# Kernel tuning notes

Hardware: AMD Instinct MI355X
Metric: run time of the kernel (lower is better)

## Reference

```python
import jax, jax.numpy as jnp
import numpy as np

B, S, D, H, F = 4, 2048, 1024, 16, 4096
HD = D // H
EPS = 1e-5


def _xavier(key, shape, fan_in, fan_out):
    a = float(np.sqrt(6.0 / (fan_in + fan_out)))
    return jax.random.uniform(key, shape, jnp.float32, -a, a)


def setup_inputs() -> dict:
    key = jax.random.key(0)
    ks = jax.random.split(key, 8)
    x = jax.random.normal(ks[0], (B, S, D), jnp.float32)
    # torch xavier_uniform on (1,H,D,HD) uses fan_in=D, fan_out=HD
    Wq = _xavier(ks[1], (H, D, HD), D, HD)
    Wk = _xavier(ks[2], (H, D, HD), D, HD)
    Wv = _xavier(ks[3], (H, D, HD), D, HD)
    Wo = _xavier(ks[4], (D, D), D, D)
    w_in = _xavier(ks[5], (D, F), D, F)
    b_in = jnp.zeros((F,), jnp.float32)
    w_out = _xavier(ks[6], (F, D), F, D)
    b_out = jnp.zeros((D,), jnp.float32)
    g1 = jnp.ones((D,), jnp.float32)
    be1 = jnp.zeros((D,), jnp.float32)
    g2 = jnp.ones((D,), jnp.float32)
    be2 = jnp.zeros((D,), jnp.float32)
    return {"x": x, "Wq": Wq, "Wk": Wk, "Wv": Wv, "Wo": Wo,
            "g1": g1, "be1": be1, "w_in": w_in, "b_in": b_in,
            "w_out": w_out, "b_out": b_out, "g2": g2, "be2": be2}


def _layernorm(x, g, b):
    mu = jnp.mean(x, axis=-1, keepdims=True)
    var = jnp.mean(jnp.square(x - mu), axis=-1, keepdims=True)
    return (x - mu) * jax.lax.rsqrt(var + EPS) * g + b


def reference(x, Wq, Wk, Wv, Wo, g1, be1, w_in, b_in, w_out, b_out, g2, be2):
    b, s, d = x.shape
    h, _, hd = Wq.shape
    q = jnp.einsum('bsd,hde->bhse', x, Wq)
    k = jnp.einsum('bsd,hde->bhse', x, Wk)
    v = jnp.einsum('bsd,hde->bhse', x, Wv)
    scores = jnp.einsum('bhse,bhte->bhst', q, k) / jnp.sqrt(jnp.float32(hd))
    causal = jnp.triu(jnp.ones((s, s), bool), k=1)  # [S,S]
    scores = jnp.where(causal, -jnp.inf, scores)
    p = jax.nn.softmax(scores, axis=-1)
    attn = jnp.einsum('bhst,bhte->bhse', p, v)
    # torch .view on contiguous (B,H,S,hd) -> (B,S,H*hd): plain reshape (no transpose)
    attn = attn.reshape(b, s, h * hd)
    attn = attn @ Wo
    x = _layernorm(x + attn, g1, be1)
    ffn = jax.nn.relu(x @ w_in + b_in) @ w_out + b_out
    x = _layernorm(x + ffn, g2, be2)
    return x
```

## Files before the change

### kernel.cpp

```cpp
#include <hip/hip_runtime.h>
#include <hip/hip_bf16.h>

typedef __hip_bfloat16 bf16;

#define BB 4
#define SS 2048
#define DD 1024
#define HH 16
#define FF 4096
#define HD 64
#define LN_EPS 1e-5f
#define QSCALE 0.1803368801111204f

typedef __attribute__((ext_vector_type(8))) __bf16 bf16x8;
typedef __attribute__((ext_vector_type(8))) unsigned short u16x8;
typedef __attribute__((ext_vector_type(4))) float f32x4;

__device__ __forceinline__ float cvt(float v) { return v; }
__device__ __forceinline__ float cvt(bf16 v) { return __bfloat162float(v); }
__device__ __forceinline__ void stf(float* p, float v) { *p = v; }
__device__ __forceinline__ void stf(bf16* p, float v) { *p = __float2bfloat16(v); }

__device__ __forceinline__ unsigned short f2bf_rne(float x) {
    unsigned int u = __float_as_uint(x);
    unsigned int r = (u + 0x7fffu + ((u >> 16) & 1u)) >> 16;
    return (unsigned short)r;
}

__device__ __forceinline__ void async_cp16(const void* g, void* l) {
    __builtin_amdgcn_global_load_lds(
        (const __attribute__((address_space(1))) unsigned int*)g,
        (__attribute__((address_space(3))) unsigned int*)l, 16, 0, 0);
}

__device__ __forceinline__ u16x8 ld_f32_chunk(const float* p) {
    const float4* q = (const float4*)p;
    const float4 a = q[0], b = q[1];
    u16x8 r;
    r[0] = f2bf_rne(a.x); r[1] = f2bf_rne(a.y); r[2] = f2bf_rne(a.z); r[3] = f2bf_rne(a.w);
    r[4] = f2bf_rne(b.x); r[5] = f2bf_rne(b.y); r[6] = f2bf_rne(b.z); r[7] = f2bf_rne(b.w);
    return r;
}

template <typename TA, typename TC, int EPI>
__launch_bounds__(256)
__global__ void mfma_gemm(const TA* __restrict__ A, const bf16* __restrict__ Bt,
                          TC* __restrict__ C, const float* __restrict__ bias,
                          const bf16* __restrict__ resb,
                          bf16* __restrict__ C2, bf16* __restrict__ C3,
                          int M, int N, int K, float oscale) {
    constexpr bool AF = (sizeof(TA) == 4);
    __shared__ unsigned short As[128 * 64];
    __shared__ unsigned short Bs[128 * 64];

    const int tid = threadIdx.x;
    const int lane = tid & 63;
    const int w = tid >> 6;
    const int wm = w >> 1, wn = w & 1;
    const int m0 = blockIdx.y * 128, n0 = blockIdx.x * 128;

    int ff[4], fr[4], fc[4], fg[4];
#pragma unroll
    for (int i = 0; i < 4; ++i) {
        ff[i] = tid + i * 256;
        fr[i] = ff[i] >> 3;
        fc[i] = ff[i] & 7;
        fg[i] = fc[i] ^ (fr[i] & 7);
    }

    f32x4 acc[4][4];
#pragma unroll
    for (int i = 0; i < 4; ++i)
#pragma unroll
        for (int j = 0; j < 4; ++j) acc[i][j] = (f32x4){0.f, 0.f, 0.f, 0.f};

    u16x8 sa[4];
    if (AF) {
#pragma unroll
        for (int i = 0; i < 4; ++i)
            sa[i] = ld_f32_chunk((const float*)A + (size_t)(m0 + fr[i]) * K + fg[i] * 8);
    }

    for (int k0 = 0; k0 < K; k0 += 64) {
        if (k0 > 0) __syncthreads();
        if (AF) {
#pragma unroll
            for (int i = 0; i < 4; ++i)
                *(u16x8*)&As[ff[i] * 8] = sa[i];
        } else {
#pragma unroll
            for (int i = 0; i < 4; ++i)
                async_cp16((const unsigned short*)A + (size_t)(m0 + fr[i]) * K + k0 + fg[i] * 8,
                           &As[ff[i] * 8]);
        }
#pragma unroll
        for (int i = 0; i < 4; ++i)
            async_cp16((const unsigned short*)Bt + (size_t)(n0 + fr[i]) * K + k0 + fg[i] * 8,
                       &Bs[ff[i] * 8]);
        __syncthreads();

        if (AF && k0 + 64 < K) {
            const int kn = k0 + 64;
#pragma unroll
            for (int i = 0; i < 4; ++i)
                sa[i] = ld_f32_chunk((const float*)A + (size_t)(m0 + fr[i]) * K + kn + fg[i] * 8);
        }

#pragma unroll
        for (int ks = 0; ks < 2; ++ks) {
            bf16x8 af[4], bfr[4];
#pragma unroll
            for (int i = 0; i < 4; ++i) {
                const int row = wm * 64 + i * 16 + (lane & 15);
                const int col = wn * 64 + i * 16 + (lane & 15);
                const int g = ks * 4 + (lane >> 4);
                af[i]  = *(const bf16x8*)&As[row * 64 + (g ^ (row & 7)) * 8];
                bfr[i] = *(const bf16x8*)&Bs[col * 64 + (g ^ (col & 7)) * 8];
            }
#pragma unroll
            for (int i = 0; i < 4; ++i)
#pragma unroll
                for (int j = 0; j < 4; ++j)
                    acc[i][j] = __builtin_amdgcn_mfma_f32_16x16x32_bf16(
                        af[i], bfr[j], acc[i][j], 0, 0, 0);
        }
    }

#pragma unroll
    for (int i = 0; i < 4; ++i) {
        const int mrow0 = m0 + wm * 64 + i * 16 + (lane >> 4) * 4;
#pragma unroll
        for (int j = 0; j < 4; ++j) {
            const int n = n0 + wn * 64 + j * 16 + (lane & 15);
            if (EPI == 5) {
                const int reg = n >> 10;
                const int nn = n & 1023;
                if (reg == 0) {
#pragma unroll
                    for (int r = 0; r < 4; ++r)
                        stf((bf16*)C + (size_t)(mrow0 + r) * 1024 + nn, acc[i][j][r] * oscale);
                } else if (reg == 1) {
#pragma unroll
                    for (int r = 0; r < 4; ++r)
                        stf(C2 + (size_t)(mrow0 + r) * 1024 + nn, acc[i][j][r]);
                } else {
                    const int bb = mrow0 >> 11, s = mrow0 & 2047;
                    ushort4 pk;
                    pk.x = f2bf_rne(acc[i][j][0]);
                    pk.y = f2bf_rne(acc[i][j][1]);
                    pk.z = f2bf_rne(acc[i][j][2]);
                    pk.w = f2bf_rne(acc[i][j][3]);
                    *(ushort4*)((unsigned short*)C3 + ((size_t)bb * 1024 + nn) * SS + s) = pk;
                }
            } else {
#pragma unroll
                for (int r = 0; r < 4; ++r) {
                    const size_t idx = (size_t)(mrow0 + r) * N + n;
                    float v = acc[i][j][r];
                    if (EPI == 0) v *= oscale;
                    if (EPI == 2) { v += bias[n]; v = fmaxf(v, 0.0f); }
                    if (EPI == 6) v += bias[n] + cvt(resb[idx]);
                    if (EPI == 7) v += cvt(resb[idx]);
                    stf(&C[idx], v);
                }
            }
        }
    }
}

__launch_bounds__(256)
__global__ void tr_f32_bf16(const float* __restrict__ in, bf16* __restrict__ out,
                            int R, int C) {
    __shared__ float t[32][33];
    const size_t zo = (size_t)blockIdx.z * R * C;
    const int bx = blockIdx.x * 32;
    const int by = blockIdx.y * 32;
    const int tx = threadIdx.x & 31, ty = threadIdx.x >> 5;
#pragma unroll
    for (int i = 0; i < 32; i += 8)
        t[ty + i][tx] = in[zo + (size_t)(by + ty + i) * C + bx + tx];
    __syncthreads();
#pragma unroll
    for (int i = 0; i < 32; i += 8)
        out[zo + (size_t)(bx + ty + i) * R + by + tx] = __float2bfloat16(t[tx][ty + i]);
}

__launch_bounds__(256)
__global__ void f32_to_bf16_kernel(const float* __restrict__ in, bf16* __restrict__ out) {
    const int i = blockIdx.x * 256 + threadIdx.x;
    const float4 v = ((const float4*)in)[i];
    ushort4 p;
    p.x = f2bf_rne(v.x); p.y = f2bf_rne(v.y); p.z = f2bf_rne(v.z); p.w = f2bf_rne(v.w);
    ((ushort4*)out)[i] = p;
}

__launch_bounds__(256, 4)
__global__ void attn_mfma(const bf16* __restrict__ Q, const bf16* __restrict__ K,
                          const bf16* __restrict__ VT, bf16* __restrict__ O) {
    __shared__ unsigned short Ks[64 * 64];
    __shared__ unsigned short Vs[64 * 64];
    __shared__ unsigned short Ps[64 * 72];

    const int tid = threadIdx.x;
    const int lane = tid & 63;
    const int w = tid >> 6;
    const int ln = lane & 15;
    const int qd = lane >> 4;
    const int bh = blockIdx.x;
    const int b = bh >> 4;
    const int h = bh & 15;
    const int qi = 31 - blockIdx.y;
    const int q0 = qi * 64;

    bf16x8 aq[2];
    {
        const unsigned short* qp =
            (const unsigned short*)Q + ((size_t)b * SS + q0 + w * 16 + ln) * DD + h * HD;
#pragma unroll
        for (int ks = 0; ks < 2; ++ks)
            aq[ks] = *(const bf16x8*)(qp + ks * 32 + qd * 8);
    }

    int sf[2], sr[2], sg[2];
#pragma unroll
    for (int i = 0; i < 2; ++i) {
        sf[i] = tid + i * 256;
        sr[i] = sf[i] >> 3;
        sg[i] = (sf[i] & 7) ^ (sr[i] & 7);
    }
    const unsigned short* kbase = (const unsigned short*)K + (size_t)b * SS * DD + h * HD;
    const unsigned short* vbase = (const unsigned short*)VT + (size_t)(b * DD + h * HD) * SS;

    f32x4 oacc[4];
#pragma unroll
    for (int e = 0; e < 4; ++e) oacc[e] = (f32x4){0.f, 0.f, 0.f, 0.f};
    float l_r[4] = {0.f, 0.f, 0.f, 0.f};

    for (int kt = 0; kt <= qi; ++kt) {
        const int t0 = kt * 64;
        __syncthreads();
#pragma unroll
        for (int i = 0; i < 2; ++i) {
            async_cp16(kbase + (size_t)(t0 + sr[i]) * DD + sg[i] * 8, &Ks[sf[i] * 8]);
            async_cp16(vbase + (size_t)sr[i] * SS + t0 + sg[i] * 8, &Vs[sf[i] * 8]);
        }
        __syncthreads();

        f32x4 sfr[4];
#pragma unroll
        for (int ct = 0; ct < 4; ++ct) {
            const int row = ct * 16 + ln;
            const bf16x8 b0 = *(const bf16x8*)&Ks[row * 64 + ((qd) ^ (row & 7)) * 8];
            const bf16x8 b1 = *(const bf16x8*)&Ks[row * 64 + ((4 + qd) ^ (row & 7)) * 8];
            f32x4 t = __builtin_amdgcn_mfma_f32_16x16x32_bf16(
                aq[0], b0, (f32x4){0.f, 0.f, 0.f, 0.f}, 0, 0, 0);
            sfr[ct] = __builtin_amdgcn_mfma_f32_16x16x32_bf16(aq[1], b1, t, 0, 0, 0);
        }

        if (kt == qi) {
#pragma unroll
            for (int ct = 0; ct < 4; ++ct) {
                const int tg = t0 + ct * 16 + ln;
#pragma unroll
                for (int r = 0; r < 4; ++r) {
                    const int qg = q0 + w * 16 + qd * 4 + r;
                    if (tg > qg) sfr[ct][r] = -1e30f;
                }
            }
        }

#pragma unroll
        for (int ct = 0; ct < 4; ++ct)
#pragma unroll
            for (int r = 0; r < 4; ++r)
                sfr[ct][r] = __builtin_amdgcn_exp2f(sfr[ct][r]);
#pragma unroll
        for (int r = 0; r < 4; ++r)
            l_r[r] += (sfr[0][r] + sfr[1][r]) + (sfr[2][r] + sfr[3][r]);

#pragma unroll
        for (int ct = 0; ct < 4; ++ct)
#pragma unroll
            for (int r = 0; r < 4; ++r)
                Ps[(w * 16 + qd * 4 + r) * 72 + ct * 16 + ln] = f2bf_rne(sfr[ct][r]);
        const bf16x8 ap0 = *(const bf16x8*)&Ps[(w * 16 + ln) * 72 + qd * 8];
        const bf16x8 ap1 = *(const bf16x8*)&Ps[(w * 16 + ln) * 72 + 32 + qd * 8];

#pragma unroll
        for (int et = 0; et < 4; ++et) {
            const int row = et * 16 + ln;
            const bf16x8 v0 = *(const bf16x8*)&Vs[row * 64 + ((qd) ^ (row & 7)) * 8];
            const bf16x8 v1 = *(const bf16x8*)&Vs[row * 64 + ((4 + qd) ^ (row & 7)) * 8];
            oacc[et] = __builtin_amdgcn_mfma_f32_16x16x32_bf16(ap0, v0, oacc[et], 0, 0, 0);
            oacc[et] = __builtin_amdgcn_mfma_f32_16x16x32_bf16(ap1, v1, oacc[et], 0, 0, 0);
        }
    }

#pragma unroll
    for (int st = 1; st <= 8; st <<= 1)
#pragma unroll
        for (int r = 0; r < 4; ++r)
            l_r[r] += __shfl_xor(l_r[r], st);
    float linv[4];
#pragma unroll
    for (int r = 0; r < 4; ++r) linv[r] = 1.0f / l_r[r];
    unsigned short* ob = (unsigned short*)O + (size_t)bh * SS * HD;
#pragma unroll
    for (int et = 0; et < 4; ++et)
#pragma unroll
        for (int r = 0; r < 4; ++r) {
            const int qg = q0 + w * 16 + qd * 4 + r;
            ob[(size_t)qg * HD + et * 16 + ln] = f2bf_rne(oacc[et][r] * linv[r]);
        }
}

template <typename TIN, typename TOUT>
__launch_bounds__(256)
__global__ void ln_kernel(const TIN* __restrict__ X, TOUT* __restrict__ Y,
                          const float* __restrict__ g, const float* __restrict__ be) {
    const int row = blockIdx.x;
    const int tid = threadIdx.x;
    const int lane = tid & 63, w = tid >> 6;
    __shared__ float red[8];
    __shared__ float mv[2];

    float4 v;
    if (sizeof(TIN) == 4) {
        v = ((const float4*)((const float*)X + (size_t)row * DD))[tid];
    } else {
        const ushort4 u = ((const ushort4*)((const unsigned short*)X + (size_t)row * DD))[tid];
        v.x = __uint_as_float((unsigned)u.x << 16);
        v.y = __uint_as_float((unsigned)u.y << 16);
        v.z = __uint_as_float((unsigned)u.z << 16);
        v.w = __uint_as_float((unsigned)u.w << 16);
    }
    float s = (v.x + v.y) + (v.z + v.w);
    float q = (v.x * v.x + v.y * v.y) + (v.z * v.z + v.w * v.w);
#pragma unroll
    for (int st = 1; st < 64; st <<= 1) {
        s += __shfl_xor(s, st);
        q += __shfl_xor(q, st);
    }
    if (lane == 0) { red[w] = s; red[4 + w] = q; }
    __syncthreads();
    if (tid == 0) {
        const float ts = (red[0] + red[1]) + (red[2] + red[3]);
        const float tq = (red[4] + red[5]) + (red[6] + red[7]);
        const float mu = ts * (1.0f / DD);
        mv[0] = mu;
        mv[1] = rsqrtf(tq * (1.0f / DD) - mu * mu + LN_EPS);
    }
    __syncthreads();
    const float mu = mv[0], rs = mv[1];
    const float4 gg = ((const float4*)g)[tid];
    const float4 bb = ((const float4*)be)[tid];
    float o[4];
    o[0] = (v.x - mu) * rs * gg.x + bb.x;
    o[1] = (v.y - mu) * rs * gg.y + bb.y;
    o[2] = (v.z - mu) * rs * gg.z + bb.z;
    o[3] = (v.w - mu) * rs * gg.w + bb.w;
    if (sizeof(TOUT) == 4) {
        float4 of = {o[0], o[1], o[2], o[3]};
        ((float4*)((float*)Y + (size_t)row * DD))[tid] = of;
    } else {
        ushort4 p;
        p.x = f2bf_rne(o[0]); p.y = f2bf_rne(o[1]);
        p.z = f2bf_rne(o[2]); p.w = f2bf_rne(o[3]);
        ((ushort4*)((unsigned short*)Y + (size_t)row * DD))[tid] = p;
    }
}

extern "C" void kernel_launch(void* const* d_in, const int* in_sizes, int n_in,
                              void* d_out, int out_size, void* d_ws, size_t ws_size,
                              hipStream_t stream) {
    const float* x = (const float*)d_in[0];
    const float* Wq = (const float*)d_in[1];
    const float* Wk = (const float*)d_in[2];
    const float* Wv = (const float*)d_in[3];
    const float* Wo = (const float*)d_in[4];
    const float* g1 = (const float*)d_in[5];
    const float* be1 = (const float*)d_in[6];
    const float* w_in = (const float*)d_in[7];
    const float* b_in = (const float*)d_in[8];
    const float* w_out = (const float*)d_in[9];
    const float* b_out = (const float*)d_in[10];
    const float* g2 = (const float*)d_in[11];
    const float* be2 = (const float*)d_in[12];
    float* out = (float*)d_out;

    char* wsb = (char*)d_ws;
    const size_t MiB = 1u << 20;
    bf16* Qb = (bf16*)(wsb);
    bf16* Kb = (bf16*)(wsb + 16 * MiB);
    bf16* VT = (bf16*)(wsb + 32 * MiB);
    bf16* At = (bf16*)(wsb + 48 * MiB);
    bf16* xb = (bf16*)(wsb + 64 * MiB);
    bf16* X1b = (bf16*)(wsb + 80 * MiB);
    bf16* Hd = (bf16*)(wsb);
    bf16* X2b = (bf16*)(wsb + 64 * MiB);
    bf16* WqkvT = (bf16*)(wsb + 96 * MiB);
    bf16* WoT = (bf16*)(wsb + 102 * MiB);
    bf16* w_inT = (bf16*)(wsb + 104 * MiB);
    bf16* w_outT = (bf16*)(wsb + 112 * MiB);
    (void)ws_size;

    const int M = BB * SS;
    dim3 blk(256);

    f32_to_bf16_kernel<<<dim3(M * DD / 4 / 256), blk, 0, stream>>>(x, xb);

    tr_f32_bf16<<<dim3(2, 32, 16), blk, 0, stream>>>(Wq, WqkvT, DD, HD);
    tr_f32_bf16<<<dim3(2, 32, 16), blk, 0, stream>>>(Wk, WqkvT + (size_t)DD * DD, DD, HD);
    tr_f32_bf16<<<dim3(2, 32, 16), blk, 0, stream>>>(Wv, WqkvT + 2 * (size_t)DD * DD, DD, HD);
    tr_f32_bf16<<<dim3(32, 32, 1), blk, 0, stream>>>(Wo, WoT, DD, DD);
    tr_f32_bf16<<<dim3(128, 32, 1), blk, 0, stream>>>(w_in, w_inT, DD, FF);
    tr_f32_bf16<<<dim3(32, 128, 1), blk, 0, stream>>>(w_out, w_outT, FF, DD);

    mfma_gemm<bf16, bf16, 5><<<dim3(3 * DD / 128, M / 128), blk, 0, stream>>>(
        xb, WqkvT, Qb, nullptr, nullptr, Kb, VT, M, 3 * DD, DD, QSCALE);

    attn_mfma<<<dim3(BB * HH, SS / 64), blk, 0, stream>>>(Qb, Kb, VT, At);

    mfma_gemm<bf16, bf16, 7><<<dim3(DD / 128, M / 128), blk, 0, stream>>>(
        At, WoT, X1b, nullptr, xb, nullptr, nullptr, M, DD, DD, 1.0f);
    ln_kernel<bf16, bf16><<<dim3(M), blk, 0, stream>>>(X1b, X1b, g1, be1);

    mfma_gemm<bf16, bf16, 2><<<dim3(FF / 128, M / 128), blk, 0, stream>>>(
        X1b, w_inT, Hd, b_in, nullptr, nullptr, nullptr, M, FF, DD, 1.0f);

    mfma_gemm<bf16, bf16, 6><<<dim3(DD / 128, M / 128), blk, 0, stream>>>(
        Hd, w_outT, X2b, b_out, X1b, nullptr, nullptr, M, DD, FF, 1.0f);

    ln_kernel<bf16, float><<<dim3(M), blk, 0, stream>>>(X2b, out, g2, be2);
}
```

Measured before the change: 475.4 us.

## Process 128-key tiles per attention iteration and merge QKV weight transposes

The causal attention kernel now loads and processes 128 keys per loop iteration instead of 64. K, V and P shared buffers are widened, and the V swizzle is extended to 16 slots. This halves the number of barrier-synchronised tile loads per query block and gives more MFMA work between syncs. The cost is more shared memory (launch bounds lowered to 3 blocks) and some wasted masked work on the diagonal tile when the query tile index is even. Separately, the three per-head Q/K/V weight transposes are merged into a single kernel launch.

```diff
diff --git a/kernel.cpp b/kernel.cpp
--- a/kernel.cpp
+++ b/kernel.cpp
@@ -186,6 +186,27 @@
 }
 
 __launch_bounds__(256)
+__global__ void tr_qkv(const float* __restrict__ Wq, const float* __restrict__ Wk,
+                       const float* __restrict__ Wv, bf16* __restrict__ out) {
+    __shared__ float t[32][33];
+    const int wi = blockIdx.z >> 4;
+    const int head = blockIdx.z & 15;
+    const float* in = (wi == 0) ? Wq : (wi == 1) ? Wk : Wv;
+    const size_t in_o = (size_t)head * DD * HD;
+    const size_t out_o = (size_t)wi * DD * DD + (size_t)head * HD * DD;
+    const int bx = blockIdx.x * 32;
+    const int by = blockIdx.y * 32;
+    const int tx = threadIdx.x & 31, ty = threadIdx.x >> 5;
+#pragma unroll
+    for (int i = 0; i < 32; i += 8)
+        t[ty + i][tx] = in[in_o + (size_t)(by + ty + i) * HD + bx + tx];
+    __syncthreads();
+#pragma unroll
+    for (int i = 0; i < 32; i += 8)
+        out[out_o + (size_t)(bx + ty + i) * DD + by + tx] = __float2bfloat16(t[tx][ty + i]);
+}
+
+__launch_bounds__(256)
 __global__ void f32_to_bf16_kernel(const float* __restrict__ in, bf16* __restrict__ out) {
     const int i = blockIdx.x * 256 + threadIdx.x;
     const float4 v = ((const float4*)in)[i];
@@ -194,12 +215,12 @@
     ((ushort4*)out)[i] = p;
 }
 
-__launch_bounds__(256, 4)
+__launch_bounds__(256, 3)
 __global__ void attn_mfma(const bf16* __restrict__ Q, const bf16* __restrict__ K,
                           const bf16* __restrict__ VT, bf16* __restrict__ O) {
-    __shared__ unsigned short Ks[64 * 64];
-    __shared__ unsigned short Vs[64 * 64];
-    __shared__ unsigned short Ps[64 * 72];
+    __shared__ unsigned short Ks[128 * 64];
+    __shared__ unsigned short Vs[64 * 128];
+    __shared__ unsigned short Ps[64 * 136];
 
     const int tid = threadIdx.x;
     const int lane = tid & 63;
@@ -216,17 +237,16 @@
     {
         const unsigned short* qp =
             (const unsigned short*)Q + ((size_t)b * SS + q0 + w * 16 + ln) * DD + h * HD;
-#pragma unroll
-        for (int ks = 0; ks < 2; ++ks)
-            aq[ks] = *(const bf16x8*)(qp + ks * 32 + qd * 8);
-    }
-
-    int sf[2], sr[2], sg[2];
-#pragma unroll
-    for (int i = 0; i < 2; ++i) {
-        sf[i] = tid + i * 256;
-        sr[i] = sf[i] >> 3;
-        sg[i] = (sf[i] & 7) ^ (sr[i] & 7);
+        aq[0] = *(const bf16x8*)(qp + qd * 8);
+        aq[1] = *(const bf16x8*)(qp + 32 + qd * 8);
+    }
+
+    int kr[4], kg[4], vr[4], vg[4];
+#pragma unroll
+    for (int i = 0; i < 4; ++i) {
+        const int f = tid + i * 256;
+        kr[i] = f >> 3;  kg[i] = (f & 7) ^ (kr[i] & 7);
+        vr[i] = f >> 4;  vg[i] = (f & 15) ^ (vr[i] & 15);
     }
     const unsigned short* kbase = (const unsigned short*)K + (size_t)b * SS * DD + h * HD;
     const unsigned short* vbase = (const unsigned short*)VT + (size_t)(b * DD + h * HD) * SS;
@@ -236,19 +256,21 @@
     for (int e = 0; e < 4; ++e) oacc[e] = (f32x4){0.f, 0.f, 0.f, 0.f};
     float l_r[4] = {0.f, 0.f, 0.f, 0.f};
 
-    for (int kt = 0; kt <= qi; ++kt) {
-        const int t0 = kt * 64;
+    const int nt = (qi >> 1) + 1;
+    for (int kt = 0; kt < nt; ++kt) {
+        const int t0 = kt * 128;
         __syncthreads();
 #pragma unroll
-        for (int i = 0; i < 2; ++i) {
-            async_cp16(kbase + (size_t)(t0 + sr[i]) * DD + sg[i] * 8, &Ks[sf[i] * 8]);
-            async_cp16(vbase + (size_t)sr[i] * SS + t0 + sg[i] * 8, &Vs[sf[i] * 8]);
+        for (int i = 0; i < 4; ++i) {
+            const int f = tid + i * 256;
+            async_cp16(kbase + (size_t)(t0 + kr[i]) * DD + kg[i] * 8, &Ks[f * 8]);
+            async_cp16(vbase + (size_t)vr[i] * SS + t0 + vg[i] * 8, &Vs[f * 8]);
         }
         __syncthreads();
 
-        f32x4 sfr[4];
-#pragma unroll
-        for (int ct = 0; ct < 4; ++ct) {
+        f32x4 sfr[8];
+#pragma unroll
+        for (int ct = 0; ct < 8; ++ct) {
             const int row = ct * 16 + ln;
             const bf16x8 b0 = *(const bf16x8*)&Ks[row * 64 + ((qd) ^ (row & 7)) * 8];
             const bf16x8 b1 = *(const bf16x8*)&Ks[row * 64 + ((4 + qd) ^ (row & 7)) * 8];
@@ -257,9 +279,9 @@
             sfr[ct] = __builtin_amdgcn_mfma_f32_16x16x32_bf16(aq[1], b1, t, 0, 0, 0);
         }
 
-        if (kt == qi) {
-#pragma unroll
-            for (int ct = 0; ct < 4; ++ct) {
+        if (kt == nt - 1) {
+#pragma unroll
+            for (int ct = 0; ct < 8; ++ct) {
                 const int tg = t0 + ct * 16 + ln;
 #pragma unroll
                 for (int r = 0; r < 4; ++r) {
@@ -270,29 +292,34 @@
         }
 
 #pragma unroll
-        for (int ct = 0; ct < 4; ++ct)
+        for (int ct = 0; ct < 8; ++ct)
 #pragma unroll
             for (int r = 0; r < 4; ++r)
                 sfr[ct][r] = __builtin_amdgcn_exp2f(sfr[ct][r]);
 #pragma unroll
         for (int r = 0; r < 4; ++r)
-            l_r[r] += (sfr[0][r] + sfr[1][r]) + (sfr[2][r] + sfr[3][r]);
-
-#pragma unroll
-        for (int ct = 0; ct < 4; ++ct)
+            l_r[r] += ((sfr[0][r] + sfr[1][r]) + (sfr[2][r] + sfr[3][r])) +
+                      ((sfr[4][r] + sfr[5][r]) + (sfr[6][r] + sfr[7][r]));
+
+#pragma unroll
+        for (int ct = 0; ct < 8; ++ct)
 #pragma unroll
             for (int r = 0; r < 4; ++r)
-                Ps[(w * 16 + qd * 4 + r) * 72 + ct * 16 + ln] = f2bf_rne(sfr[ct][r]);
-        const bf16x8 ap0 = *(const bf16x8*)&Ps[(w * 16 + ln) * 72 + qd * 8];
-        const bf16x8 ap1 = *(const bf16x8*)&Ps[(w * 16 + ln) * 72 + 32 + qd * 8];
+                Ps[(w * 16 + qd * 4 + r) * 136 + ct * 16 + ln] = f2bf_rne(sfr[ct][r]);
+        bf16x8 ap[4];
+#pragma unroll
+        for (int ks = 0; ks < 4; ++ks)
+            ap[ks] = *(const bf16x8*)&Ps[(w * 16 + ln) * 136 + ks * 32 + qd * 8];
 
 #pragma unroll
         for (int et = 0; et < 4; ++et) {
             const int row = et * 16 + ln;
-            const bf16x8 v0 = *(const bf16x8*)&Vs[row * 64 + ((qd) ^ (row & 7)) * 8];
-            const bf16x8 v1 = *(const bf16x8*)&Vs[row * 64 + ((4 + qd) ^ (row & 7)) * 8];
-            oacc[et] = __builtin_amdgcn_mfma_f32_16x16x32_bf16(ap0, v0, oacc[et], 0, 0, 0);
-            oacc[et] = __builtin_amdgcn_mfma_f32_16x16x32_bf16(ap1, v1, oacc[et], 0, 0, 0);
+#pragma unroll
+            for (int ks = 0; ks < 4; ++ks) {
+                const int slot = (ks * 4 + qd) ^ (row & 15);
+                const bf16x8 v = *(const bf16x8*)&Vs[row * 128 + slot * 8];
+                oacc[et] = __builtin_amdgcn_mfma_f32_16x16x32_bf16(ap[ks], v, oacc[et], 0, 0, 0);
+            }
         }
     }
 
@@ -409,9 +436,7 @@
 
     f32_to_bf16_kernel<<<dim3(M * DD / 4 / 256), blk, 0, stream>>>(x, xb);
 
-    tr_f32_bf16<<<dim3(2, 32, 16), blk, 0, stream>>>(Wq, WqkvT, DD, HD);
-    tr_f32_bf16<<<dim3(2, 32, 16), blk, 0, stream>>>(Wk, WqkvT + (size_t)DD * DD, DD, HD);
-    tr_f32_bf16<<<dim3(2, 32, 16), blk, 0, stream>>>(Wv, WqkvT + 2 * (size_t)DD * DD, DD, HD);
+    tr_qkv<<<dim3(2, 32, 48), blk, 0, stream>>>(Wq, Wk, Wv, WqkvT);
     tr_f32_bf16<<<dim3(32, 32, 1), blk, 0, stream>>>(Wo, WoT, DD, DD);
     tr_f32_bf16<<<dim3(128, 32, 1), blk, 0, stream>>>(w_in, w_inT, DD, FF);
     tr_f32_bf16<<<dim3(32, 128, 1), blk, 0, stream>>>(w_out, w_outT, FF, DD);
```

Measured after the change: 479.6 us. About the same (+0.9%).
